# Kernel optimization log

Measured on AMD Instinct MI355X. Metric: run time of the kernel, lower is better.

## Reference

```python
import jax, jax.numpy as jnp
import numpy as np

B, C, IMG = 128, 3, 224
P = 16
NP = (IMG // P) ** 2          # 196 patches
S = 1 + NP                    # 197 tokens
D = 384
HEADS = 6
HD = D // HEADS               # 64
DEPTH = 12
HID = 4 * D                   # 1536
NCLS = 100
PATCH_DIM = C * P * P         # 768
EPS = 1e-5


def setup_inputs() -> dict:
    key = jax.random.key(0)
    ks = jax.random.split(key, 24)
    g = lambda k, shape, s=0.02: jax.random.normal(k, shape, dtype=jnp.float32) * s
    return {
        "x": jax.random.normal(ks[0], (B, C, IMG, IMG), dtype=jnp.float32),
        "patch_w": g(ks[1], (D, PATCH_DIM)),
        "patch_b": jnp.zeros((D,), jnp.float32),
        "cls_token": g(ks[2], (1, 1, D)),
        "pos_embed": g(ks[3], (1, S, D)),
        "ln1_g": jnp.ones((DEPTH, D), jnp.float32),
        "ln1_b": jnp.zeros((DEPTH, D), jnp.float32),
        "qkv_w": g(ks[4], (DEPTH, 3 * D, D)),
        "qkv_b": jnp.zeros((DEPTH, 3 * D), jnp.float32),
        "out_w": g(ks[5], (DEPTH, D, D)),
        "out_b": jnp.zeros((DEPTH, D), jnp.float32),
        "ln2_g": jnp.ones((DEPTH, D), jnp.float32),
        "ln2_b": jnp.zeros((DEPTH, D), jnp.float32),
        "fc1_w": g(ks[6], (DEPTH, HID, D)),
        "fc1_b": jnp.zeros((DEPTH, HID), jnp.float32),
        "fc2_w": g(ks[7], (DEPTH, D, HID)),
        "fc2_b": jnp.zeros((DEPTH, D), jnp.float32),
        "lnf_g": jnp.ones((D,), jnp.float32),
        "lnf_b": jnp.zeros((D,), jnp.float32),
        "head_w": g(ks[8], (NCLS, D)),
    }


def _ln(x, g, b):
    m = jnp.mean(x, axis=-1, keepdims=True)
    v = jnp.mean(jnp.square(x - m), axis=-1, keepdims=True)
    return (x - m) * jax.lax.rsqrt(v + EPS) * g + b


def reference(x, patch_w, patch_b, cls_token, pos_embed,
              ln1_g, ln1_b, qkv_w, qkv_b, out_w, out_b,
              ln2_g, ln2_b, fc1_w, fc1_b, fc2_w, fc2_b,
              lnf_g, lnf_b, head_w):
    b = x.shape[0]
    hp = IMG // P
    # patchify: unfold(2,P).unfold(3,P).permute(0,2,3,1,4,5) -> [B, N, C*P*P]
    patches = x.reshape(b, C, hp, P, hp, P).transpose(0, 2, 4, 1, 3, 5).reshape(b, NP, PATCH_DIM)
    tok = patches @ patch_w.T + patch_b                           # [B, NP, D]
    h = jnp.concatenate([jnp.broadcast_to(cls_token, (b, 1, D)), tok], axis=1)
    h = h + pos_embed[:, :S, :]
    scale = 1.0 / np.sqrt(HD).astype(np.float32)
    for i in range(DEPTH):
        xn = _ln(h, ln1_g[i], ln1_b[i])
        qkv = xn @ qkv_w[i].T + qkv_b[i]                          # [B, S, 3D]
        q, k, v = jnp.split(qkv, 3, axis=-1)
        q = q.reshape(b, S, HEADS, HD).transpose(0, 2, 1, 3) * scale
        k = k.reshape(b, S, HEADS, HD).transpose(0, 2, 1, 3)
        v = v.reshape(b, S, HEADS, HD).transpose(0, 2, 1, 3)
        attn = jax.nn.softmax(jnp.einsum('bhqd,bhkd->bhqk', q, k), axis=-1)
        ctx = jnp.einsum('bhqk,bhkd->bhqd', attn, v)
        ctx = ctx.transpose(0, 2, 1, 3).reshape(b, S, D)
        h = h + (ctx @ out_w[i].T + out_b[i])
        xn2 = _ln(h, ln2_g[i], ln2_b[i])
        hid = jax.nn.gelu(xn2 @ fc1_w[i].T + fc1_b[i], approximate=False)
        h = h + (hid @ fc2_w[i].T + fc2_b[i])
    cls = _ln(h[:, 0], lnf_g, lnf_b)
    return cls @ head_w.T                                         # [B, NCLS]
```

## Files before the change

### kernel.cpp

```cpp
#include <hip/hip_runtime.h>
#include <hip/hip_bf16.h>


#define S_ 197
#define D_ 384
#define BATCH 128

using bf16 = __hip_bfloat16;
typedef __attribute__((ext_vector_type(8))) __bf16 bf16x8;
typedef __attribute__((ext_vector_type(4))) float f32x4;

#if __has_builtin(__builtin_amdgcn_global_load_lds)
#define HAVE_GLL 1
__device__ __forceinline__ void gll16(const bf16* g, __bf16* l) {
  __builtin_amdgcn_global_load_lds(
      (const __attribute__((address_space(1))) void*)g,
      (__attribute__((address_space(3))) void*)l, 16, 0, 0);
}
#else
#define HAVE_GLL 0
#endif

__global__ __launch_bounds__(256) void k_f2b(const float* __restrict__ src,
                                             bf16* __restrict__ dst, int n4) {
  int i = blockIdx.x * 256 + threadIdx.x;
  if (i >= n4) return;
  float4 v = ((const float4*)src)[i];
  bf16 o[4] = {__float2bfloat16(v.x), __float2bfloat16(v.y),
               __float2bfloat16(v.z), __float2bfloat16(v.w)};
  ((uint2*)dst)[i] = *(uint2*)o;
}

__global__ __launch_bounds__(256) void k_embed_init(const float* __restrict__ cls,
                                                    const float* __restrict__ pos,
                                                    float* __restrict__ h) {
  int idx = blockIdx.x * 256 + threadIdx.x;
  if (idx >= BATCH * S_ * D_) return;
  int d = idx % D_;
  int s = (idx / D_) % S_;
  float v = pos[s * D_ + d];
  if (s == 0) v += cls[d];
  h[idx] = v;
}

__global__ __launch_bounds__(256) void k_patchify(const float* __restrict__ x,
                                                  bf16* __restrict__ patches) {
  int idx = blockIdx.x * 256 + threadIdx.x;
  if (idx >= BATCH * 196 * 768) return;
  int f = idx % 768;
  int n = (idx / 768) % 196;
  int b = idx / (768 * 196);
  int c = f >> 8, rem = f & 255, dy = rem >> 4, dx = rem & 15;
  int py = n / 14, px = n % 14;
  patches[idx] = __float2bfloat16(
      x[(((size_t)b * 3 + c) * 224 + py * 16 + dy) * 224 + px * 16 + dx]);
}

template <int MODE>
__global__ __launch_bounds__(256, 4) void k_gemm(const bf16* __restrict__ X,
                                                 const bf16* __restrict__ W,
                                                 const float* __restrict__ bias,
                                                 bf16* __restrict__ out,
                                                 float* __restrict__ res,
                                                 int N, int K, int remap) {
  __shared__ __align__(16) __bf16 As[2][128 * 32];
  __shared__ __align__(16) __bf16 Bs[2][128 * 32];
  const int tid = threadIdx.x;
  const int m0 = blockIdx.y * 128, n0 = blockIdx.x * 128;
  const int lane = tid & 63, w = tid >> 6;
  const int wr = w >> 1, wc = w & 1;
  const int l16 = lane & 15, quad = lane >> 4;
  f32x4 acc[4][4] = {};

  const int srow = w * 32 + (lane >> 2);
  const int scol = (((lane & 3) ^ ((lane >> 3) & 3)) << 3);
  const bf16* Ag = X + (size_t)(m0 + srow) * K + scol;
  const bf16* Bg = W + (size_t)(n0 + srow) * K + scol;
  const int ldsW = w * 32 * 32;

  const int jx8 = ((quad ^ ((l16 >> 1) & 3)) << 3);
  const int aoff = (wr * 64 + l16) * 32 + jx8;
  const int boff = (wc * 64 + l16) * 32 + jx8;

#if HAVE_GLL
#define STAGE(buf, k0)                                         \
  do {                                                         \
    gll16(Ag + (k0), &As[buf][ldsW]);                          \
    gll16(Ag + (k0) + (size_t)16 * K, &As[buf][ldsW + 512]);   \
    gll16(Bg + (k0), &Bs[buf][ldsW]);                          \
    gll16(Bg + (k0) + (size_t)16 * K, &Bs[buf][ldsW + 512]);   \
  } while (0)
#else
#define STAGE(buf, k0)                                                        \
  do {                                                                        \
    *(uint4*)(&As[buf][ldsW + (lane >> 2) * 32 + (lane & 3) * 8]) =           \
        *(const uint4*)(Ag + (k0));                                           \
    *(uint4*)(&As[buf][ldsW + 512 + (lane >> 2) * 32 + (lane & 3) * 8]) =     \
        *(const uint4*)(Ag + (k0) + (size_t)16 * K);                          \
    *(uint4*)(&Bs[buf][ldsW + (lane >> 2) * 32 + (lane & 3) * 8]) =           \
        *(const uint4*)(Bg + (k0));                                           \
    *(uint4*)(&Bs[buf][ldsW + 512 + (lane >> 2) * 32 + (lane & 3) * 8]) =     \
        *(const uint4*)(Bg + (k0) + (size_t)16 * K);                          \
  } while (0)
#endif

  STAGE(0, 0);
  __syncthreads();
  for (int k0 = 0; k0 < K; k0 += 32) {
    const int cb = (k0 >> 5) & 1;
    if (k0 + 32 < K) STAGE(cb ^ 1, k0 + 32);
    bf16x8 av[4], bv[4];
#pragma unroll
    for (int i = 0; i < 4; i++)
      av[i] = *(const bf16x8*)(&As[cb][aoff + i * 512]);
#pragma unroll
    for (int j = 0; j < 4; j++)
      bv[j] = *(const bf16x8*)(&Bs[cb][boff + j * 512]);
#pragma unroll
    for (int i = 0; i < 4; i++)
#pragma unroll
      for (int j = 0; j < 4; j++)
        acc[i][j] = __builtin_amdgcn_mfma_f32_16x16x32_bf16(av[i], bv[j], acc[i][j], 0, 0, 0);
    __syncthreads();
  }
#undef STAGE

  float bvv[4];
#pragma unroll
  for (int j = 0; j < 4; j++)
    bvv[j] = bias[n0 + wc * 64 + j * 16 + l16];
#pragma unroll
  for (int i = 0; i < 4; i++) {
    const int rbase = m0 + wr * 64 + i * 16 + quad * 4;
#pragma unroll
    for (int j = 0; j < 4; j++) {
      const int col = n0 + wc * 64 + j * 16 + l16;
#pragma unroll
      for (int r = 0; r < 4; r++) {
        float v = acc[i][j][r] + bvv[j];
        int rw = rbase + r;
        if (MODE == 0) {
          out[(size_t)rw * N + col] = __float2bfloat16(v);
        } else if (MODE == 1) {
          float gl = 0.5f * v * (1.f + erff(v * 0.70710678118f));
          out[(size_t)rw * N + col] = __float2bfloat16(gl);
        } else {
          int hr = remap ? (rw + rw / 196 + 1) : rw;
          res[(size_t)hr * N + col] += v;
        }
      }
    }
  }
}

__global__ __launch_bounds__(128) void k_ln(const float* __restrict__ h,
                                            const float* __restrict__ g,
                                            const float* __restrict__ bt,
                                            bf16* __restrict__ xn) {
  const int r = blockIdx.x, t = threadIdx.x;
  const float* row = h + (size_t)r * D_;
  float x0 = row[t], x1 = row[t + 128], x2 = row[t + 256];
  float s = x0 + x1 + x2;
  float q = x0 * x0 + x1 * x1 + x2 * x2;
#pragma unroll
  for (int o = 32; o; o >>= 1) {
    s += __shfl_xor(s, o);
    q += __shfl_xor(q, o);
  }
  __shared__ float rs[2], rq[2];
  if ((t & 63) == 0) { rs[t >> 6] = s; rq[t >> 6] = q; }
  __syncthreads();
  s = rs[0] + rs[1];
  q = rq[0] + rq[1];
  const float mean = s * (1.f / 384.f);
  const float var = q * (1.f / 384.f) - mean * mean;
  const float rstd = rsqrtf(var + 1e-5f);
  bf16* o = xn + (size_t)r * D_;
  o[t] = __float2bfloat16((x0 - mean) * rstd * g[t] + bt[t]);
  o[t + 128] = __float2bfloat16((x1 - mean) * rstd * g[t + 128] + bt[t + 128]);
  o[t + 256] = __float2bfloat16((x2 - mean) * rstd * g[t + 256] + bt[t + 256]);
}

__global__ __launch_bounds__(256) void k_attn(const bf16* __restrict__ qkv,
                                              bf16* __restrict__ ctx) {
  const int bh = blockIdx.x;
  const int b = bh / 6, hd = bh % 6;
  const bf16* Qg = qkv + (size_t)b * S_ * 1152 + hd * 64;
  const bf16* Kg = Qg + 384;
  const bf16* Vg = Qg + 768;
  __shared__ __align__(16) __bf16 Vt[64 * 232];
  __shared__ __align__(16) __bf16 Ps[4][16 * 232];
  const int tid = threadIdx.x;
  const int lane = tid & 63, w = tid >> 6;
  const int l16 = lane & 15, quad = lane >> 4;
  const __bf16 z = (__bf16)0.0f;

  for (int i = tid; i < 64 * 35; i += 256) {
    int d = i / 35, k = 197 + i % 35;
    Vt[d * 232 + k] = z;
  }
  for (int i = tid; i < S_ * 64; i += 256) {
    int k = i >> 6, d = i & 63;
    Vt[d * 232 + k] = *(const __bf16*)&Vg[(size_t)k * 1152 + d];
  }
  for (int i = lane; i < 16 * 24; i += 64) {
    int r = i / 24, c = 208 + i % 24;
    Ps[w][r * 232 + c] = z;
  }
  __syncthreads();

  const bf16x8 zf = {};
  for (int band = w; band < 13; band += 4) {
    const int qrow = band * 16 + l16;
    bf16x8 aq0 = zf, aq1 = zf;
    if (qrow < S_) {
      aq0 = *(const bf16x8*)(Qg + (size_t)qrow * 1152 + quad * 8);
      aq1 = *(const bf16x8*)(Qg + (size_t)qrow * 1152 + 32 + quad * 8);
    }
    f32x4 sc[13];
#pragma unroll
    for (int t = 0; t < 13; t++) {
      const int krow = t * 16 + l16;
      bf16x8 bk0 = zf, bk1 = zf;
      if (krow < S_) {
        bk0 = *(const bf16x8*)(Kg + (size_t)krow * 1152 + quad * 8);
        bk1 = *(const bf16x8*)(Kg + (size_t)krow * 1152 + 32 + quad * 8);
      }
      f32x4 a = {};
      a = __builtin_amdgcn_mfma_f32_16x16x32_bf16(aq0, bk0, a, 0, 0, 0);
      a = __builtin_amdgcn_mfma_f32_16x16x32_bf16(aq1, bk1, a, 0, 0, 0);
      sc[t] = a;
    }
#pragma unroll
    for (int t = 0; t < 13; t++)
#pragma unroll
      for (int r = 0; r < 4; r++) sc[t][r] *= 0.125f;
    if (l16 >= 5) {
#pragma unroll
      for (int r = 0; r < 4; r++) sc[12][r] = -1e30f;
    }
    f32x4 mx = sc[0];
#pragma unroll
    for (int t = 1; t < 13; t++)
#pragma unroll
      for (int r = 0; r < 4; r++) mx[r] = fmaxf(mx[r], sc[t][r]);
#pragma unroll
    for (int o = 1; o < 16; o <<= 1)
#pragma unroll
      for (int r = 0; r < 4; r++) mx[r] = fmaxf(mx[r], __shfl_xor(mx[r], o));
    f32x4 sum = {};
#pragma unroll
    for (int t = 0; t < 13; t++)
#pragma unroll
      for (int r = 0; r < 4; r++) {
        float p = __expf(sc[t][r] - mx[r]);
        sc[t][r] = p;
        sum[r] += p;
      }
#pragma unroll
    for (int o = 1; o < 16; o <<= 1)
#pragma unroll
      for (int r = 0; r < 4; r++) sum[r] += __shfl_xor(sum[r], o);
    f32x4 rinv;
#pragma unroll
    for (int r = 0; r < 4; r++) rinv[r] = 1.0f / sum[r];
#pragma unroll
    for (int t = 0; t < 13; t++)
#pragma unroll
      for (int r = 0; r < 4; r++)
        Ps[w][(quad * 4 + r) * 232 + t * 16 + l16] = (__bf16)sc[t][r];
    f32x4 oacc[4] = {};
#pragma unroll
    for (int ks = 0; ks < 7; ks++) {
      bf16x8 pa = *(const bf16x8*)&Ps[w][l16 * 232 + ks * 32 + quad * 8];
#pragma unroll
      for (int c = 0; c < 4; c++) {
        bf16x8 bv = *(const bf16x8*)&Vt[(c * 16 + l16) * 232 + ks * 32 + quad * 8];
        oacc[c] = __builtin_amdgcn_mfma_f32_16x16x32_bf16(pa, bv, oacc[c], 0, 0, 0);
      }
    }
    const int orow = band * 16 + quad * 4;
#pragma unroll
    for (int c = 0; c < 4; c++)
#pragma unroll
      for (int r = 0; r < 4; r++) {
        const int rw = orow + r;
        if (rw < S_)
          ctx[((size_t)b * S_ + rw) * D_ + hd * 64 + c * 16 + l16] =
              __float2bfloat16(oacc[c][r] * rinv[r]);
      }
  }
}

__global__ __launch_bounds__(128) void k_head(const float* __restrict__ h,
                                              const float* __restrict__ g,
                                              const float* __restrict__ bt,
                                              const float* __restrict__ hw,
                                              float* __restrict__ out) {
  const int b = blockIdx.x, t = threadIdx.x;
  const float* row = h + (size_t)b * S_ * D_;
  float x0 = row[t], x1 = row[t + 128], x2 = row[t + 256];
  float s = x0 + x1 + x2;
  float q = x0 * x0 + x1 * x1 + x2 * x2;
#pragma unroll
  for (int o = 32; o; o >>= 1) {
    s += __shfl_xor(s, o);
    q += __shfl_xor(q, o);
  }
  __shared__ float rs[2], rq[2];
  if ((t & 63) == 0) { rs[t >> 6] = s; rq[t >> 6] = q; }
  __syncthreads();
  s = rs[0] + rs[1];
  q = rq[0] + rq[1];
  const float mean = s * (1.f / 384.f);
  const float var = q * (1.f / 384.f) - mean * mean;
  const float rstd = rsqrtf(var + 1e-5f);
  __shared__ float clsn[384];
  clsn[t] = (x0 - mean) * rstd * g[t] + bt[t];
  clsn[t + 128] = (x1 - mean) * rstd * g[t + 128] + bt[t + 128];
  clsn[t + 256] = (x2 - mean) * rstd * g[t + 256] + bt[t + 256];
  __syncthreads();
  if (t < 100) {
    const float* wr = hw + (size_t)t * D_;
    float a = 0.f;
    for (int d = 0; d < 384; d++) a += clsn[d] * wr[d];
    out[b * 100 + t] = a;
  }
}

extern "C" void kernel_launch(void* const* d_in, const int* in_sizes, int n_in,
                              void* d_out, int out_size, void* d_ws, size_t ws_size,
                              hipStream_t stream) {
  (void)in_sizes; (void)n_in; (void)out_size; (void)ws_size;
  const float* x       = (const float*)d_in[0];
  const float* patch_w = (const float*)d_in[1];
  const float* patch_b = (const float*)d_in[2];
  const float* cls_tok = (const float*)d_in[3];
  const float* pos_emb = (const float*)d_in[4];
  const float* ln1_g   = (const float*)d_in[5];
  const float* ln1_b   = (const float*)d_in[6];
  const float* qkv_w   = (const float*)d_in[7];
  const float* qkv_b   = (const float*)d_in[8];
  const float* out_w   = (const float*)d_in[9];
  const float* out_b   = (const float*)d_in[10];
  const float* ln2_g   = (const float*)d_in[11];
  const float* ln2_b   = (const float*)d_in[12];
  const float* fc1_w   = (const float*)d_in[13];
  const float* fc1_b   = (const float*)d_in[14];
  const float* fc2_w   = (const float*)d_in[15];
  const float* fc2_b   = (const float*)d_in[16];
  const float* lnf_g   = (const float*)d_in[17];
  const float* lnf_b   = (const float*)d_in[18];
  const float* head_w  = (const float*)d_in[19];
  float* out = (float*)d_out;

  const size_t R = (size_t)BATCH * S_;
  char* p = (char*)d_ws;
  float* h  = (float*)p; p += R * 384 * 4;
  bf16* xn  = (bf16*)p;  p += R * 384 * 2;
  bf16* u   = (bf16*)p;  p += R * 1536 * 2;
  bf16* qkvb = u;
  bf16* ctxb = u + R * 1152;
  bf16* hidb = u;
  bf16* patches = u;
  bf16* wb  = (bf16*)p;
  bf16* patch_wb = wb;
  bf16* qkv_wb   = patch_wb + 294912;
  bf16* out_wb   = qkv_wb + 5308416;
  bf16* fc1_wb   = out_wb + 1769472;
  bf16* fc2_wb   = fc1_wb + 7077888;

  k_f2b<<<dim3((294912 / 4 + 255) / 256), dim3(256), 0, stream>>>(patch_w, patch_wb, 294912 / 4);
  k_f2b<<<dim3((5308416 / 4 + 255) / 256), dim3(256), 0, stream>>>(qkv_w, qkv_wb, 5308416 / 4);
  k_f2b<<<dim3((1769472 / 4 + 255) / 256), dim3(256), 0, stream>>>(out_w, out_wb, 1769472 / 4);
  k_f2b<<<dim3((7077888 / 4 + 255) / 256), dim3(256), 0, stream>>>(fc1_w, fc1_wb, 7077888 / 4);
  k_f2b<<<dim3((7077888 / 4 + 255) / 256), dim3(256), 0, stream>>>(fc2_w, fc2_wb, 7077888 / 4);

  k_embed_init<<<dim3((BATCH * S_ * D_) / 256), dim3(256), 0, stream>>>(cls_tok, pos_emb, h);
  k_patchify<<<dim3((BATCH * 196 * 768) / 256), dim3(256), 0, stream>>>(x, patches);
  k_gemm<2><<<dim3(3, 196), dim3(256), 0, stream>>>(patches, patch_wb, patch_b, nullptr, h, 384, 768, 1);

  for (int i = 0; i < 12; i++) {
    k_ln<<<dim3((unsigned)R), dim3(128), 0, stream>>>(h, ln1_g + i * 384, ln1_b + i * 384, xn);
    k_gemm<0><<<dim3(9, 197), dim3(256), 0, stream>>>(xn, qkv_wb + (size_t)i * 1152 * 384,
                                                      qkv_b + i * 1152, qkvb, nullptr, 1152, 384, 0);
    k_attn<<<dim3(768), dim3(256), 0, stream>>>(qkvb, ctxb);
    k_gemm<2><<<dim3(3, 197), dim3(256), 0, stream>>>(ctxb, out_wb + (size_t)i * 384 * 384,
                                                      out_b + i * 384, nullptr, h, 384, 384, 0);
    k_ln<<<dim3((unsigned)R), dim3(128), 0, stream>>>(h, ln2_g + i * 384, ln2_b + i * 384, xn);
    k_gemm<1><<<dim3(12, 197), dim3(256), 0, stream>>>(xn, fc1_wb + (size_t)i * 1536 * 384,
                                                       fc1_b + i * 1536, hidb, nullptr, 1536, 384, 0);
    k_gemm<2><<<dim3(3, 197), dim3(256), 0, stream>>>(hidb, fc2_wb + (size_t)i * 384 * 1536,
                                                      fc2_b + i * 384, nullptr, h, 384, 1536, 0);
  }
  k_head<<<dim3(128), dim3(128), 0, stream>>>(h, lnf_g, lnf_b, head_w, out);
}
```

Measured before the change: 3.713 ms.

## Fuse LayerNorm into QKV and FC1 GEMM prologues, folding gamma/beta into weights

Removes the standalone LayerNorm kernels. Gamma is folded into the bf16 weight conversion and beta into a precomputed bias via W·beta. The QKV and FC1 GEMMs now compute per-row mean and rstd from the fp32 residual in a prologue, then normalize while staging A into LDS. This drops the xn bf16 round trip and two launches per layer, but each N-tile block recomputes row statistics and reads fp32 A through registers instead of the direct global-to-LDS path.

Measured after the change: 5.073 ms. 1.37x slower.

```diff
diff --git a/kernel.cpp b/kernel.cpp
--- a/kernel.cpp
+++ b/kernel.cpp
@@ -29,6 +29,41 @@
   bf16 o[4] = {__float2bfloat16(v.x), __float2bfloat16(v.y),
                __float2bfloat16(v.z), __float2bfloat16(v.w)};
   ((uint2*)dst)[i] = *(uint2*)o;
+}
+
+__global__ __launch_bounds__(256) void k_f2b_g(const float* __restrict__ src,
+                                               const float* __restrict__ g,
+                                               bf16* __restrict__ dst, int n4,
+                                               int rowsPerLayer) {
+  int i = blockIdx.x * 256 + threadIdx.x;
+  if (i >= n4) return;
+  size_t base = (size_t)i * 4;
+  int col = (int)(base % 384);
+  int layer = (int)(base / ((size_t)rowsPerLayer * 384));
+  float4 v = ((const float4*)src)[i];
+  float4 gg = *(const float4*)(g + (size_t)layer * 384 + col);
+  bf16 o[4] = {__float2bfloat16(v.x * gg.x), __float2bfloat16(v.y * gg.y),
+               __float2bfloat16(v.z * gg.z), __float2bfloat16(v.w * gg.w)};
+  ((uint2*)dst)[i] = *(uint2*)o;
+}
+
+__global__ __launch_bounds__(256) void k_biasfold(const float* __restrict__ W,
+                                                  const float* __restrict__ lnb,
+                                                  const float* __restrict__ base,
+                                                  float* __restrict__ outb,
+                                                  int rowsPerLayer) {
+  int n = blockIdx.x * 256 + threadIdx.x;
+  if (n >= 12 * rowsPerLayer) return;
+  int layer = n / rowsPerLayer, r = n % rowsPerLayer;
+  const float* wr = W + ((size_t)layer * rowsPerLayer + r) * 384;
+  const float* bb = lnb + (size_t)layer * 384;
+  float a = base[n];
+  for (int k = 0; k < 384; k += 4) {
+    float4 wv = *(const float4*)(wr + k);
+    float4 bv = *(const float4*)(bb + k);
+    a += wv.x * bv.x + wv.y * bv.y + wv.z * bv.z + wv.w * bv.w;
+  }
+  outb[n] = a;
 }
 
 __global__ __launch_bounds__(256) void k_embed_init(const float* __restrict__ cls,
@@ -56,15 +91,15 @@
       x[(((size_t)b * 3 + c) * 224 + py * 16 + dy) * 224 + px * 16 + dx]);
 }
 
-template <int MODE>
-__global__ __launch_bounds__(256, 4) void k_gemm(const bf16* __restrict__ X,
-                                                 const bf16* __restrict__ W,
-                                                 const float* __restrict__ bias,
-                                                 bf16* __restrict__ out,
-                                                 float* __restrict__ res,
-                                                 int N, int K, int remap) {
+template <int MODE, int LNF>
+__global__ __launch_bounds__(256, 4) void k_gemm(
+    const bf16* __restrict__ X, const bf16* __restrict__ W,
+    const float* __restrict__ bias, bf16* __restrict__ out,
+    float* __restrict__ res, const float* __restrict__ Xf,
+    int N, int K, int remap) {
   __shared__ __align__(16) __bf16 As[2][128 * 32];
   __shared__ __align__(16) __bf16 Bs[2][128 * 32];
+  __shared__ float smean[128], srstd[128];
   const int tid = threadIdx.x;
   const int m0 = blockIdx.y * 128, n0 = blockIdx.x * 128;
   const int lane = tid & 63, w = tid >> 6;
@@ -74,29 +109,92 @@
 
   const int srow = w * 32 + (lane >> 2);
   const int scol = (((lane & 3) ^ ((lane >> 3) & 3)) << 3);
-  const bf16* Ag = X + (size_t)(m0 + srow) * K + scol;
+  const bf16* Ag = LNF ? nullptr : X + (size_t)(m0 + srow) * K + scol;
   const bf16* Bg = W + (size_t)(n0 + srow) * K + scol;
   const int ldsW = w * 32 * 32;
+
+  const float* hA = nullptr;
+  float mA0 = 0.f, rA0 = 0.f, mA1 = 0.f, rA1 = 0.f;
+  if constexpr (LNF) {
+    for (int rr = 0; rr < 4; rr++) {
+      const int r = w * 32 + rr * 8 + (lane >> 3);
+      const float* hr = Xf + (size_t)(m0 + r) * 384 + (lane & 7) * 48;
+      float s = 0.f, q = 0.f;
+#pragma unroll
+      for (int c = 0; c < 12; c++) {
+        float4 v = ((const float4*)hr)[c];
+        s += v.x + v.y + v.z + v.w;
+        q += v.x * v.x + v.y * v.y + v.z * v.z + v.w * v.w;
+      }
+#pragma unroll
+      for (int o = 1; o < 8; o <<= 1) {
+        s += __shfl_xor(s, o);
+        q += __shfl_xor(q, o);
+      }
+      if ((lane & 7) == 0) {
+        float m = s * (1.f / 384.f);
+        smean[r] = m;
+        srstd[r] = rsqrtf(q * (1.f / 384.f) - m * m + 1e-5f);
+      }
+    }
+    __syncthreads();
+    hA = Xf + (size_t)(m0 + srow) * 384 + scol;
+    mA0 = smean[srow];      rA0 = srstd[srow];
+    mA1 = smean[srow + 16]; rA1 = srstd[srow + 16];
+  }
 
   const int jx8 = ((quad ^ ((l16 >> 1) & 3)) << 3);
   const int aoff = (wr * 64 + l16) * 32 + jx8;
   const int boff = (wc * 64 + l16) * 32 + jx8;
 
+  auto stageA_ln = [&](int buf, int k0) {
+    float4 u0 = *(const float4*)(hA + k0);
+    float4 u1 = *(const float4*)(hA + k0 + 4);
+    float4 v0 = *(const float4*)(hA + 16 * 384 + k0);
+    float4 v1 = *(const float4*)(hA + 16 * 384 + k0 + 4);
+    bf16 t0[8] = {__float2bfloat16((u0.x - mA0) * rA0),
+                  __float2bfloat16((u0.y - mA0) * rA0),
+                  __float2bfloat16((u0.z - mA0) * rA0),
+                  __float2bfloat16((u0.w - mA0) * rA0),
+                  __float2bfloat16((u1.x - mA0) * rA0),
+                  __float2bfloat16((u1.y - mA0) * rA0),
+                  __float2bfloat16((u1.z - mA0) * rA0),
+                  __float2bfloat16((u1.w - mA0) * rA0)};
+    bf16 t1[8] = {__float2bfloat16((v0.x - mA1) * rA1),
+                  __float2bfloat16((v0.y - mA1) * rA1),
+                  __float2bfloat16((v0.z - mA1) * rA1),
+                  __float2bfloat16((v0.w - mA1) * rA1),
+                  __float2bfloat16((v1.x - mA1) * rA1),
+                  __float2bfloat16((v1.y - mA1) * rA1),
+                  __float2bfloat16((v1.z - mA1) * rA1),
+                  __float2bfloat16((v1.w - mA1) * rA1)};
+    *(uint4*)(&As[buf][ldsW + (lane >> 2) * 32 + (lane & 3) * 8]) = *(uint4*)t0;
+    *(uint4*)(&As[buf][ldsW + 512 + (lane >> 2) * 32 + (lane & 3) * 8]) = *(uint4*)t1;
+  };
+
 #if HAVE_GLL
-#define STAGE(buf, k0)                                         \
-  do {                                                         \
-    gll16(Ag + (k0), &As[buf][ldsW]);                          \
-    gll16(Ag + (k0) + (size_t)16 * K, &As[buf][ldsW + 512]);   \
-    gll16(Bg + (k0), &Bs[buf][ldsW]);                          \
-    gll16(Bg + (k0) + (size_t)16 * K, &Bs[buf][ldsW + 512]);   \
+#define STAGE(buf, k0)                                           \
+  do {                                                           \
+    if constexpr (LNF) {                                         \
+      stageA_ln(buf, k0);                                        \
+    } else {                                                     \
+      gll16(Ag + (k0), &As[buf][ldsW]);                          \
+      gll16(Ag + (k0) + (size_t)16 * K, &As[buf][ldsW + 512]);   \
+    }                                                            \
+    gll16(Bg + (k0), &Bs[buf][ldsW]);                            \
+    gll16(Bg + (k0) + (size_t)16 * K, &Bs[buf][ldsW + 512]);     \
   } while (0)
 #else
 #define STAGE(buf, k0)                                                        \
   do {                                                                        \
-    *(uint4*)(&As[buf][ldsW + (lane >> 2) * 32 + (lane & 3) * 8]) =           \
-        *(const uint4*)(Ag + (k0));                                           \
-    *(uint4*)(&As[buf][ldsW + 512 + (lane >> 2) * 32 + (lane & 3) * 8]) =     \
-        *(const uint4*)(Ag + (k0) + (size_t)16 * K);                          \
+    if constexpr (LNF) {                                                      \
+      stageA_ln(buf, k0);                                                     \
+    } else {                                                                  \
+      *(uint4*)(&As[buf][ldsW + (lane >> 2) * 32 + (lane & 3) * 8]) =         \
+          *(const uint4*)(Ag + (k0));                                         \
+      *(uint4*)(&As[buf][ldsW + 512 + (lane >> 2) * 32 + (lane & 3) * 8]) =   \
+          *(const uint4*)(Ag + (k0) + (size_t)16 * K);                        \
+    }                                                                         \
     *(uint4*)(&Bs[buf][ldsW + (lane >> 2) * 32 + (lane & 3) * 8]) =           \
         *(const uint4*)(Bg + (k0));                                           \
     *(uint4*)(&Bs[buf][ldsW + 512 + (lane >> 2) * 32 + (lane & 3) * 8]) =     \
@@ -151,34 +249,6 @@
       }
     }
   }
-}
-
-__global__ __launch_bounds__(128) void k_ln(const float* __restrict__ h,
-                                            const float* __restrict__ g,
-                                            const float* __restrict__ bt,
-                                            bf16* __restrict__ xn) {
-  const int r = blockIdx.x, t = threadIdx.x;
-  const float* row = h + (size_t)r * D_;
-  float x0 = row[t], x1 = row[t + 128], x2 = row[t + 256];
-  float s = x0 + x1 + x2;
-  float q = x0 * x0 + x1 * x1 + x2 * x2;
-#pragma unroll
-  for (int o = 32; o; o >>= 1) {
-    s += __shfl_xor(s, o);
-    q += __shfl_xor(q, o);
-  }
-  __shared__ float rs[2], rq[2];
-  if ((t & 63) == 0) { rs[t >> 6] = s; rq[t >> 6] = q; }
-  __syncthreads();
-  s = rs[0] + rs[1];
-  q = rq[0] + rq[1];
-  const float mean = s * (1.f / 384.f);
-  const float var = q * (1.f / 384.f) - mean * mean;
-  const float rstd = rsqrtf(var + 1e-5f);
-  bf16* o = xn + (size_t)r * D_;
-  o[t] = __float2bfloat16((x0 - mean) * rstd * g[t] + bt[t]);
-  o[t + 128] = __float2bfloat16((x1 - mean) * rstd * g[t + 128] + bt[t + 128]);
-  o[t + 256] = __float2bfloat16((x2 - mean) * rstd * g[t + 256] + bt[t + 256]);
 }
 
 __global__ __launch_bounds__(256) void k_attn(const bf16* __restrict__ qkv,
@@ -357,7 +427,6 @@
   const size_t R = (size_t)BATCH * S_;
   char* p = (char*)d_ws;
   float* h  = (float*)p; p += R * 384 * 4;
-  bf16* xn  = (bf16*)p;  p += R * 384 * 2;
   bf16* u   = (bf16*)p;  p += R * 1536 * 2;
   bf16* qkvb = u;
   bf16* ctxb = u + R * 1152;
@@ -369,29 +438,37 @@
   bf16* out_wb   = qkv_wb + 5308416;
   bf16* fc1_wb   = out_wb + 1769472;
   bf16* fc2_wb   = fc1_wb + 7077888;
+  p = (char*)(fc2_wb + 7077888);
+  float* qkv_bf = (float*)p; p += 12 * 1152 * 4;
+  float* fc1_bf = (float*)p;
 
   k_f2b<<<dim3((294912 / 4 + 255) / 256), dim3(256), 0, stream>>>(patch_w, patch_wb, 294912 / 4);
-  k_f2b<<<dim3((5308416 / 4 + 255) / 256), dim3(256), 0, stream>>>(qkv_w, qkv_wb, 5308416 / 4);
+  k_f2b_g<<<dim3((5308416 / 4 + 255) / 256), dim3(256), 0, stream>>>(qkv_w, ln1_g, qkv_wb, 5308416 / 4, 1152);
   k_f2b<<<dim3((1769472 / 4 + 255) / 256), dim3(256), 0, stream>>>(out_w, out_wb, 1769472 / 4);
-  k_f2b<<<dim3((7077888 / 4 + 255) / 256), dim3(256), 0, stream>>>(fc1_w, fc1_wb, 7077888 / 4);
+  k_f2b_g<<<dim3((7077888 / 4 + 255) / 256), dim3(256), 0, stream>>>(fc1_w, ln2_g, fc1_wb, 7077888 / 4, 1536);
   k_f2b<<<dim3((7077888 / 4 + 255) / 256), dim3(256), 0, stream>>>(fc2_w, fc2_wb, 7077888 / 4);
+  k_biasfold<<<dim3((12 * 1152 + 255) / 256), dim3(256), 0, stream>>>(qkv_w, ln1_b, qkv_b, qkv_bf, 1152);
+  k_biasfold<<<dim3((12 * 1536 + 255) / 256), dim3(256), 0, stream>>>(fc1_w, ln2_b, fc1_b, fc1_bf, 1536);
 
   k_embed_init<<<dim3((BATCH * S_ * D_) / 256), dim3(256), 0, stream>>>(cls_tok, pos_emb, h);
   k_patchify<<<dim3((BATCH * 196 * 768) / 256), dim3(256), 0, stream>>>(x, patches);
-  k_gemm<2><<<dim3(3, 196), dim3(256), 0, stream>>>(patches, patch_wb, patch_b, nullptr, h, 384, 768, 1);
+  k_gemm<2, 0><<<dim3(3, 196), dim3(256), 0, stream>>>(patches, patch_wb, patch_b, nullptr, h,
+                                                       nullptr, 384, 768, 1);
 
   for (int i = 0; i < 12; i++) {
-    k_ln<<<dim3((unsigned)R), dim3(128), 0, stream>>>(h, ln1_g + i * 384, ln1_b + i * 384, xn);
-    k_gemm<0><<<dim3(9, 197), dim3(256), 0, stream>>>(xn, qkv_wb + (size_t)i * 1152 * 384,
-                                                      qkv_b + i * 1152, qkvb, nullptr, 1152, 384, 0);
+    k_gemm<0, 1><<<dim3(9, 197), dim3(256), 0, stream>>>(nullptr, qkv_wb + (size_t)i * 1152 * 384,
+                                                         qkv_bf + i * 1152, qkvb, nullptr, h,
+                                                         1152, 384, 0);
     k_attn<<<dim3(768), dim3(256), 0, stream>>>(qkvb, ctxb);
-    k_gemm<2><<<dim3(3, 197), dim3(256), 0, stream>>>(ctxb, out_wb + (size_t)i * 384 * 384,
-                                                      out_b + i * 384, nullptr, h, 384, 384, 0);
-    k_ln<<<dim3((unsigned)R), dim3(128), 0, stream>>>(h, ln2_g + i * 384, ln2_b + i * 384, xn);
-    k_gemm<1><<<dim3(12, 197), dim3(256), 0, stream>>>(xn, fc1_wb + (size_t)i * 1536 * 384,
-                                                       fc1_b + i * 1536, hidb, nullptr, 1536, 384, 0);
-    k_gemm<2><<<dim3(3, 197), dim3(256), 0, stream>>>(hidb, fc2_wb + (size_t)i * 384 * 1536,
-                                                      fc2_b + i * 384, nullptr, h, 384, 1536, 0);
+    k_gemm<2, 0><<<dim3(3, 197), dim3(256), 0, stream>>>(ctxb, out_wb + (size_t)i * 384 * 384,
+                                                         out_b + i * 384, nullptr, h, nullptr,
+                                                         384, 384, 0);
+    k_gemm<1, 1><<<dim3(12, 197), dim3(256), 0, stream>>>(nullptr, fc1_wb + (size_t)i * 1536 * 384,
+                                                          fc1_bf + i * 1536, hidb, nullptr, h,
+                                                          1536, 384, 0);
+    k_gemm<2, 0><<<dim3(3, 197), dim3(256), 0, stream>>>(hidb, fc2_wb + (size_t)i * 384 * 1536,
+                                                         fc2_b + i * 384, nullptr, h, nullptr,
+                                                         384, 1536, 0);
   }
   k_head<<<dim3(128), dim3(128), 0, stream>>>(h, lnf_g, lnf_b, head_w, out);
 }
```
